# Optimization experiments

Measured on AMD Instinct MI355X. Metric: run time of the kernel, lower is better.

The kernel has to match this reference:

```python
import jax, jax.numpy as jnp
import numpy as np

NUM_CLASSES = [5, 7, 4, 6, 3, 8, 5, 4, 6, 7, 3, 5, 4, 6, 8, 5, 7, 4, 6, 3]
N_ONE_HOTS = 20
N_OTHERS = 30
H = 48
W = 48
B = 128
N_MAP = 32
ENC_OUT = 32
RES_C = 128
OH_EMB = 9
SUM_NC = sum(NUM_CLASSES)  # 106


def conv2d(x, w, b=None, pad=0):
    # x: NCHW, w: OIHW
    y = jax.lax.conv_general_dilated(
        x, w, window_strides=(1, 1), padding=[(pad, pad), (pad, pad)],
        dimension_numbers=('NCHW', 'OIHW', 'NCHW'))
    if b is not None:
        y = y + b[None, :, None, None]
    return y


def setup_inputs() -> dict:
    key = jax.random.key(0)
    ks = jax.random.split(key, 20)
    x = jax.random.normal(ks[0], (B, 1 + N_MAP, H, W), dtype=jnp.float32)
    # first N_ONE_HOTS entries of flattened channel 0 are categorical indices
    idx_cols = [jax.random.randint(jax.random.fold_in(ks[1], j), (B,), 0, nc)
                for j, nc in enumerate(NUM_CLASSES)]
    idx = jnp.stack(idx_cols, axis=1).astype(jnp.float32)  # (B, 20)
    x = x.at[:, 0, 0, :N_ONE_HOTS].set(idx)
    s = 0.05
    inp = {
        'x': x,
        'fc_w': jax.random.normal(ks[2], (OH_EMB, SUM_NC), jnp.float32) * s,
        'fc_b': jnp.zeros((OH_EMB,), jnp.float32),
        'oh_conv_w': jax.random.normal(ks[3], (OH_EMB, OH_EMB, 1, 1), jnp.float32) * s,
        'oh_conv_b': jnp.zeros((OH_EMB,), jnp.float32),
        'others_conv_w': jax.random.normal(ks[4], (N_OTHERS, N_OTHERS, 1, 1), jnp.float32) * s,
        'others_conv_b': jnp.zeros((N_OTHERS,), jnp.float32),
        'all_conv_w': jax.random.normal(ks[5], (ENC_OUT, OH_EMB + N_OTHERS, 1, 1), jnp.float32) * s,
        'all_conv_b': jnp.zeros((ENC_OUT,), jnp.float32),
        'conv1_w': jax.random.normal(ks[6], (RES_C, ENC_OUT + N_MAP, 1, 1), jnp.float32) * s,
        'conv1_b': jnp.zeros((RES_C,), jnp.float32),
        'rconv1_w': jax.random.normal(ks[7], (RES_C, RES_C, 5, 5), jnp.float32) * s,
        'rconv1_b': jnp.zeros((RES_C,), jnp.float32),
        'rconv2_w': jax.random.normal(ks[8], (RES_C, RES_C, 5, 5), jnp.float32) * s,
        'rconv2_b': jnp.zeros((RES_C,), jnp.float32),
        'se_w1': jax.random.normal(ks[9], (RES_C // 16, RES_C), jnp.float32) * s,
        'se_w2': jax.random.normal(ks[10], (RES_C, RES_C // 16), jnp.float32) * s,
    }
    return inp


def reference(x, fc_w, fc_b, oh_conv_w, oh_conv_b, others_conv_w, others_conv_b,
              all_conv_w, all_conv_b, conv1_w, conv1_b, rconv1_w, rconv1_b,
              rconv2_w, rconv2_b, se_w1, se_w2):
    b = x.shape[0]
    gi = x[:, 0].reshape(b, -1)                 # (b, H*W)
    map_feature = x[:, 1:]                      # (b, N_MAP, H, W)
    idx = jax.lax.stop_gradient(gi[:, :N_ONE_HOTS]).astype(jnp.int32)
    others = gi[:, N_ONE_HOTS:N_ONE_HOTS + N_OTHERS]   # (b, 30)
    # vectorized one-hot build (replaces the quadratic python loop)
    oh = jnp.concatenate(
        [jax.nn.one_hot(idx[:, j], nc, dtype=x.dtype) for j, nc in enumerate(NUM_CLASSES)],
        axis=1)                                 # (b, SUM_NC)
    v = oh @ fc_w.T + fc_b                      # (b, 9)
    # faithful torch expand((h,w)+shape).reshape((b,-1,h,w)) semantics
    v = jnp.broadcast_to(v, (H, W, b, OH_EMB)).reshape(b, OH_EMB, H, W)
    o = jnp.broadcast_to(others, (H, W, b, N_OTHERS)).reshape(b, N_OTHERS, H, W)
    v = conv2d(v, oh_conv_w, oh_conv_b)
    o = conv2d(o, others_conv_w, others_conv_b)
    gi_map = conv2d(jnp.concatenate([v, o], axis=1), all_conv_w, all_conv_b)  # (b, 32, H, W)
    h = conv2d(jnp.concatenate([gi_map, map_feature], axis=1), conv1_w, conv1_b)  # (b, 128, H, W)
    # residual block: 5x5 convs, LeakyReLU, SE, identity skip (in==out)
    identity = h
    y = jax.nn.leaky_relu(conv2d(h, rconv1_w, rconv1_b, pad=2))
    y = conv2d(y, rconv2_w, rconv2_b, pad=2)
    s = y.mean(axis=(2, 3))                     # (b, 128)
    s = jax.nn.sigmoid(jax.nn.relu(s @ se_w1.T) @ se_w2.T)
    y = y * s[:, :, None, None]
    return jax.nn.leaky_relu(y + identity)
```

## Files before the change

### kernel.cpp

```cpp
#include <hip/hip_runtime.h>
#include <hip/hip_bf16.h>
#include <cstddef>

#define HH 48
#define WW 48
#define PIX 2304
#define PPIX 2704
#define BB 128
#define RESC 128
#define XCH 33

typedef short bf16x8 __attribute__((ext_vector_type(8)));
typedef float f32x4 __attribute__((ext_vector_type(4)));

static __device__ __forceinline__ float b2f(unsigned short u) {
    unsigned x = ((unsigned)u) << 16;
    return __builtin_bit_cast(float, x);
}
static __device__ __forceinline__ unsigned short f2b(float f) {
    __hip_bfloat16 hb = __float2bfloat16(f);
    return __builtin_bit_cast(unsigned short, hb);
}

#define GLOAD_LDS16(gp, lp) __builtin_amdgcn_global_load_lds( \
    (const __attribute__((address_space(1))) void*)(gp), \
    (__attribute__((address_space(3))) void*)(lp), 16, 0, 0)

__global__ __launch_bounds__(256) void k_compute_G(
        const float* __restrict__ x, const float* __restrict__ fc_w,
        const float* __restrict__ fc_b,
        const float* __restrict__ ohw, const float* __restrict__ ohb,
        const float* __restrict__ otw, const float* __restrict__ otb,
        const float* __restrict__ aw,  const float* __restrict__ ab,
        const float* __restrict__ c1w, const float* __restrict__ c1b,
        float* __restrict__ G) {
    __shared__ float vsh[128][9];
    int t = threadIdx.x;
    if (t < 128) {
        const int off[20] = {0,5,12,16,22,25,33,38,42,48,55,58,63,67,73,81,86,93,97,103};
        const float* gi = x + (size_t)t * XCH * PIX;
        int cols[20];
        #pragma unroll
        for (int j = 0; j < 20; j++) cols[j] = off[j] + (int)gi[j];
        #pragma unroll
        for (int e = 0; e < 9; e++) {
            float acc = fc_b[e];
            #pragma unroll
            for (int j = 0; j < 20; j++) acc += fc_w[e * 106 + cols[j]];
            vsh[t][e] = acc;
        }
    }
    __syncthreads();
    int p = blockIdx.x * 64 + (t & 63);
    int og = t >> 6;
    if (p >= PIX) return;
    float sv = vsh[(p / 9) & 127][p % 9];
    float om[30];
    #pragma unroll
    for (int c2 = 0; c2 < 30; c2++) {
        int tmp = c2 * 24 + p;
        int c = tmp % 30;
        int bb = (c2 * 76 + tmp / 30) & 127;
        om[c2] = x[(size_t)bb * XCH * PIX + 20 + c];
    }
    float v9[9];
    #pragma unroll
    for (int e = 0; e < 9; e++) {
        float srow = 0.f;
        #pragma unroll
        for (int e2 = 0; e2 < 9; e2++) srow += ohw[e * 9 + e2];
        v9[e] = ohb[e] + srow * sv;
    }
    float o30[30];
    #pragma unroll
    for (int c = 0; c < 30; c++) {
        float a = otb[c];
        #pragma unroll
        for (int c2 = 0; c2 < 30; c2++) a += otw[c * 30 + c2] * om[c2];
        o30[c] = a;
    }
    float gi32[32];
    #pragma unroll
    for (int g = 0; g < 32; g++) {
        float a = ab[g];
        #pragma unroll
        for (int e = 0; e < 9; e++) a += aw[g * 39 + e] * v9[e];
        #pragma unroll
        for (int c = 0; c < 30; c++) a += aw[g * 39 + 9 + c] * o30[c];
        gi32[g] = a;
    }
    for (int oc = og * 32; oc < og * 32 + 32; oc++) {
        float a = c1b[oc];
        #pragma unroll
        for (int g = 0; g < 32; g++) a += c1w[oc * 64 + g] * gi32[g];
        G[p * 128 + oc] = a;
    }
}

__global__ void k_convert_w(const float* __restrict__ w1, const float* __restrict__ w2,
                            __hip_bfloat16* __restrict__ wb1, __hip_bfloat16* __restrict__ wb2) {
    int i = blockIdx.x * 256 + threadIdx.x;
    if (i >= 25 * 128 * 128) return;
    int tap = i / 16384, r = i % 16384;
    int oc = r >> 7, ic = r & 127;
    size_t src = (size_t)(oc * 128 + ic) * 25 + tap;
    wb1[i] = __float2bfloat16(w1[src]);
    wb2[i] = __float2bfloat16(w2[src]);
}

__global__ void k_zero_border(__hip_bfloat16* __restrict__ a, __hip_bfloat16* __restrict__ b2,
                              float* __restrict__ mean) {
    int img = blockIdx.x, t = threadIdx.x;
    if (t < 128) mean[img * 128 + t] = 0.f;
    for (int j = t; j < 6400; j += 256) {
        int pb = j >> 4, c16 = j & 15;
        int y, x2;
        if (pb < 208) { int q = pb / 52; y = q < 2 ? q : q + 48; x2 = pb % 52; }
        else { int r = pb - 208; y = 2 + (r >> 2); int c = r & 3; x2 = c < 2 ? c : c + 48; }
        size_t off = ((size_t)img * PPIX + y * 52 + x2) * 128 + c16 * 8;
        uint4 z = {0, 0, 0, 0};
        *(uint4*)(a + off) = z;
        *(uint4*)(b2 + off) = z;
    }
}

__global__ __launch_bounds__(256) void k_conv1(const float* __restrict__ x, const float* __restrict__ c1w,
                                               const float* __restrict__ G, __hip_bfloat16* __restrict__ h) {
    int b = blockIdx.y, p0 = blockIdx.x * 64;
    int t = threadIdx.x, wave = t >> 6, lane = t & 63;
    int l15 = lane & 15, lg = lane >> 4;

    bf16x8 a[2];
    #pragma unroll
    for (int m = 0; m < 2; ++m) {
        int oc = wave * 32 + m * 16 + l15;
        const float* wp = c1w + oc * 64 + 32 + lg * 8;
        float4 f0 = *(const float4*)wp;
        float4 f1 = *(const float4*)(wp + 4);
        unsigned short u[8] = { f2b(f0.x), f2b(f0.y), f2b(f0.z), f2b(f0.w),
                                f2b(f1.x), f2b(f1.y), f2b(f1.z), f2b(f1.w) };
        a[m] = __builtin_bit_cast(bf16x8, *(uint4*)u);
    }

    f32x4 acc[2][4] = {};
    #pragma unroll
    for (int n = 0; n < 4; ++n) {
        int p = p0 + n * 16 + l15;
        unsigned short ub[8];
        #pragma unroll
        for (int j = 0; j < 8; ++j)
            ub[j] = f2b(x[((size_t)b * XCH + 1 + lg * 8 + j) * PIX + p]);
        bf16x8 Bv = __builtin_bit_cast(bf16x8, *(uint4*)ub);
        acc[0][n] = __builtin_amdgcn_mfma_f32_16x16x32_bf16(a[0], Bv, acc[0][n], 0, 0, 0);
        acc[1][n] = __builtin_amdgcn_mfma_f32_16x16x32_bf16(a[1], Bv, acc[1][n], 0, 0, 0);
    }

    #pragma unroll
    for (int m = 0; m < 2; ++m) {
        #pragma unroll
        for (int n = 0; n < 4; ++n) {
            int oc4 = wave * 32 + m * 16 + lg * 4;
            int p = p0 + n * 16 + l15;
            int py = p / 48, px2 = p % 48;
            float4 g = *(const float4*)&G[(size_t)p * 128 + oc4];
            float v0 = acc[m][n][0] + g.x, v1 = acc[m][n][1] + g.y;
            float v2 = acc[m][n][2] + g.z, v3 = acc[m][n][3] + g.w;
            uint2 pk;
            pk.x = (unsigned)f2b(v0) | ((unsigned)f2b(v1) << 16);
            pk.y = (unsigned)f2b(v2) | ((unsigned)f2b(v3) << 16);
            *(uint2*)(&h[((size_t)b * PPIX + (py + 2) * 52 + px2 + 2) * 128 + oc4]) = pk;
        }
    }
}

template<bool LEAKY, bool MEAN, bool PADOUT>
__global__ __launch_bounds__(256, 2) void k_conv5_mfma(
        const __hip_bfloat16* __restrict__ in,
        const __hip_bfloat16* __restrict__ w,
        const float* __restrict__ bias,
        __hip_bfloat16* __restrict__ out,
        float* __restrict__ mean) {
    __shared__ __align__(16) char lds[2][25600];
    int bid = blockIdx.x;
    int xcd = bid & 7, loc = bid >> 3;
    int b = xcd * 16 + loc / 9;
    int tile = loc % 9;
    int ty0 = (tile / 3) * 16, tx0 = (tile % 3) * 16;
    int t = threadIdx.x;
    int wave = t >> 6, lane = t & 63;
    int wm = wave & 1, wn = wave >> 1;
    int l15 = lane & 15, lg = lane >> 4;

    const size_t inb = (size_t)b * PPIX * 128;
    const __hip_bfloat16* wbase = w + (size_t)(wm * 64 + l15) * 128 + lg * 8;

    int sbase[8];
    #pragma unroll
    for (int n = 0; n < 8; ++n) sbase[n] = (wn * 8 + n) * 20 + l15;

    f32x4 acc[4][8] = {};

    auto stage_part = [&](int buf, int icb2, int part) {
        int sg = part * 256 + t;
        if (sg < 1600) {
            int u = sg >> 3, j = sg & 7;
            int bb2 = j ^ (u & 7);
            int s = (u << 1) | (bb2 >> 2);
            int lg2 = bb2 & 3;
            int ry = s / 20, rx = s % 20;
            const __hip_bfloat16* gp = in + inb + (size_t)((ty0 + ry) * 52 + tx0 + rx) * 128 + icb2 + lg2 * 8;
            char* lp = &lds[buf][sg * 16];
            GLOAD_LDS16(gp, lp);
        }
    };

#define AISSUE(Areg, tap_) do { \
        const __hip_bfloat16* wp = wbase + (size_t)(tap_) * 16384 + icb; \
        Areg[0] = *(const bf16x8*)(wp); \
        Areg[1] = *(const bf16x8*)(wp + 2048); \
        Areg[2] = *(const bf16x8*)(wp + 4096); \
        Areg[3] = *(const bf16x8*)(wp + 6144); \
    } while (0)

#define LDSB(s_) (*(const bf16x8*)(cb + (((s_) >> 1) << 7) + \
        ((((((s_) & 1) << 2) | lg) ^ (((s_) >> 1) & 7)) << 4)))

#define CTAP(Areg, tap_) do { \
        int toff = (tap_) + 15 * ((tap_) / 5); \
        bf16x8 Bc0 = LDSB(sbase[0] + toff); \
        bf16x8 Bc1 = LDSB(sbase[1] + toff); \
        __builtin_amdgcn_s_setprio(1); \
        _Pragma("unroll") \
        for (int n = 0; n < 8; ++n) { \
            bf16x8 Bc2 = Bc1; \
            if (n < 6) Bc2 = LDSB(sbase[n + 2] + toff); \
            acc[0][n] = __builtin_amdgcn_mfma_f32_16x16x32_bf16(Areg[0], Bc0, acc[0][n], 0, 0, 0); \
            acc[1][n] = __builtin_amdgcn_mfma_f32_16x16x32_bf16(Areg[1], Bc0, acc[1][n], 0, 0, 0); \
            acc[2][n] = __builtin_amdgcn_mfma_f32_16x16x32_bf16(Areg[2], Bc0, acc[2][n], 0, 0, 0); \
            acc[3][n] = __builtin_amdgcn_mfma_f32_16x16x32_bf16(Areg[3], Bc0, acc[3][n], 0, 0, 0); \
            Bc0 = Bc1; Bc1 = Bc2; \
        } \
        __builtin_amdgcn_s_setprio(0); \
    } while (0)

    #pragma unroll
    for (int j = 0; j < 7; ++j) stage_part(0, 0, j);
    __syncthreads();

    for (int c = 0; c < 4; ++c) {
        const int icb = c * 32;
        const char* cb = lds[c & 1];
        bf16x8 A0[4], A1[4];
        AISSUE(A0, 0);
        AISSUE(A1, 1);
        __builtin_amdgcn_sched_barrier(0);
        for (int i = 0; i < 12; ++i) {
            int tp = 2 * i;
            CTAP(A0, tp);
            AISSUE(A0, tp + 2);
            if (c < 3 && i < 7) {
                stage_part((c + 1) & 1, icb + 32, i);
                __builtin_amdgcn_sched_barrier(0);
            }
            CTAP(A1, tp + 1);
            AISSUE(A1, tp + 3);
        }
        CTAP(A0, 24);
        if (c < 3) __syncthreads();
    }
#undef AISSUE
#undef LDSB
#undef CTAP

    #pragma unroll
    for (int m = 0; m < 4; ++m) {
        int ocm = wm * 64 + m * 16 + lg * 4;
        float bv0 = bias[ocm], bv1 = bias[ocm + 1], bv2 = bias[ocm + 2], bv3 = bias[ocm + 3];
        float ps0 = 0, ps1 = 0, ps2 = 0, ps3 = 0;
        #pragma unroll
        for (int n = 0; n < 8; ++n) {
            float v0 = acc[m][n][0] + bv0, v1 = acc[m][n][1] + bv1;
            float v2 = acc[m][n][2] + bv2, v3 = acc[m][n][3] + bv3;
            ps0 += v0; ps1 += v1; ps2 += v2; ps3 += v3;
            if (LEAKY) {
                v0 = v0 > 0.f ? v0 : 0.01f * v0; v1 = v1 > 0.f ? v1 : 0.01f * v1;
                v2 = v2 > 0.f ? v2 : 0.01f * v2; v3 = v3 > 0.f ? v3 : 0.01f * v3;
            }
            int row = ty0 + wn * 8 + n, col = tx0 + l15;
            size_t off;
            if (PADOUT) off = ((size_t)b * PPIX + (row + 2) * 52 + col + 2) * 128 + ocm;
            else        off = ((size_t)b * PIX + row * 48 + col) * 128 + ocm;
            uint2 pk;
            pk.x = (unsigned)f2b(v0) | ((unsigned)f2b(v1) << 16);
            pk.y = (unsigned)f2b(v2) | ((unsigned)f2b(v3) << 16);
            *(uint2*)(out + off) = pk;
        }
        if (MEAN) {
            #pragma unroll
            for (int mask = 1; mask < 16; mask <<= 1) {
                ps0 += __shfl_xor(ps0, mask);
                ps1 += __shfl_xor(ps1, mask);
                ps2 += __shfl_xor(ps2, mask);
                ps3 += __shfl_xor(ps3, mask);
            }
            if (l15 == 0) {
                atomicAdd(&mean[b * 128 + ocm], ps0);
                atomicAdd(&mean[b * 128 + ocm + 1], ps1);
                atomicAdd(&mean[b * 128 + ocm + 2], ps2);
                atomicAdd(&mean[b * 128 + ocm + 3], ps3);
            }
        }
    }
}

__global__ void k_se(const float* __restrict__ mean, const float* __restrict__ w1,
                     const float* __restrict__ w2, float* __restrict__ s) {
    __shared__ float m[128];
    __shared__ float tt[8];
    int b = blockIdx.x, t = threadIdx.x;
    m[t] = mean[b * RESC + t] * (1.0f / 2304.0f);
    __syncthreads();
    if (t < 8) {
        float a = 0.f;
        for (int i = 0; i < 128; i++) a += w1[t * 128 + i] * m[i];
        tt[t] = a > 0.f ? a : 0.f;
    }
    __syncthreads();
    float a = 0.f;
    #pragma unroll
    for (int r = 0; r < 8; r++) a += w2[t * 8 + r] * tt[r];
    s[b * RESC + t] = 1.f / (1.f + expf(-a));
}

__global__ __launch_bounds__(256) void k_final(const __hip_bfloat16* __restrict__ y2,
                                               const __hip_bfloat16* __restrict__ h,
                                               const float* __restrict__ sg, float* __restrict__ out) {
    __shared__ float sl[128];
    __shared__ float tile[64 * 129];
    int b = blockIdx.y, p0 = blockIdx.x * 64, t = threadIdx.x;
    if (t < 128) sl[t] = sg[b * 128 + t];
    __syncthreads();
    #pragma unroll
    for (int k = 0; k < 4; ++k) {
        int j = t + k * 256;
        int pix = j >> 4, c = j & 15;
        int p = p0 + pix;
        int py = p / 48, px2 = p % 48;
        uint4 yv = *(const uint4*)(y2 + ((size_t)b * PIX + p) * 128 + c * 8);
        uint4 hv = *(const uint4*)(h + ((size_t)b * PPIX + (py + 2) * 52 + px2 + 2) * 128 + c * 8);
        const unsigned short* yp = (const unsigned short*)&yv;
        const unsigned short* hp = (const unsigned short*)&hv;
        #pragma unroll
        for (int jj = 0; jj < 8; ++jj) {
            int oc = c * 8 + jj;
            tile[pix * 129 + oc] = b2f(yp[jj]) * sl[oc] + b2f(hp[jj]);
        }
    }
    __syncthreads();
    int oc = t >> 1, xh = (t & 1) * 32;
    float ov[32];
    #pragma unroll
    for (int i = 0; i < 32; ++i) {
        float v = tile[(xh + i) * 129 + oc];
        ov[i] = v > 0.f ? v : 0.01f * v;
    }
    float* op = out + ((size_t)b * 128 + oc) * PIX + p0 + xh;
    #pragma unroll
    for (int q = 0; q < 8; ++q) ((float4*)op)[q] = *(float4*)&ov[q * 4];
}

extern "C" void kernel_launch(void* const* d_in, const int* in_sizes, int n_in,
                              void* d_out, int out_size, void* d_ws, size_t ws_size,
                              hipStream_t stream) {
    const float* x      = (const float*)d_in[0];
    const float* fc_w   = (const float*)d_in[1];
    const float* fc_b   = (const float*)d_in[2];
    const float* ohw    = (const float*)d_in[3];
    const float* ohb    = (const float*)d_in[4];
    const float* otw    = (const float*)d_in[5];
    const float* otb    = (const float*)d_in[6];
    const float* aw     = (const float*)d_in[7];
    const float* ab     = (const float*)d_in[8];
    const float* c1w    = (const float*)d_in[9];
    const float* c1b    = (const float*)d_in[10];
    const float* r1w    = (const float*)d_in[11];
    const float* r1b    = (const float*)d_in[12];
    const float* r2w    = (const float*)d_in[13];
    const float* r2b    = (const float*)d_in[14];
    const float* se_w1  = (const float*)d_in[15];
    const float* se_w2  = (const float*)d_in[16];

    const size_t padb = (size_t)BB * PPIX * 128 * sizeof(__hip_bfloat16);
    char* ws = (char*)d_ws;
    __hip_bfloat16* h    = (__hip_bfloat16*)ws;  ws += padb;
    __hip_bfloat16* y1   = (__hip_bfloat16*)ws;  ws += padb;
    __hip_bfloat16* y2   = (__hip_bfloat16*)ws;  ws += (size_t)BB * PIX * 128 * sizeof(__hip_bfloat16);
    float* G    = (float*)ws;                    ws += (size_t)PIX * 128 * sizeof(float);
    __hip_bfloat16* wb1 = (__hip_bfloat16*)ws;   ws += (size_t)25 * 128 * 128 * sizeof(__hip_bfloat16);
    __hip_bfloat16* wb2 = (__hip_bfloat16*)ws;   ws += (size_t)25 * 128 * 128 * sizeof(__hip_bfloat16);
    ws += 262144;
    float* mean = (float*)ws;                    ws += (size_t)BB * RESC * sizeof(float);
    float* sgate= (float*)ws;                    ws += (size_t)BB * RESC * sizeof(float);

    k_compute_G<<<36, 256, 0, stream>>>(x, fc_w, fc_b, ohw, ohb, otw, otb, aw, ab, c1w, c1b, G);
    k_convert_w<<<1600, 256, 0, stream>>>(r1w, r2w, wb1, wb2);
    k_zero_border<<<128, 256, 0, stream>>>(h, y1, mean);
    k_conv1<<<dim3(36, 128), 256, 0, stream>>>(x, c1w, G, h);
    k_conv5_mfma<true, false, true><<<dim3(1152), 256, 0, stream>>>(h, wb1, r1b, y1, nullptr);
    k_conv5_mfma<false, true, false><<<dim3(1152), 256, 0, stream>>>(y1, wb2, r2b, y2, mean);
    k_se<<<128, 128, 0, stream>>>(mean, se_w1, se_w2, sgate);
    k_final<<<dim3(36, 128), 256, 0, stream>>>(y2, h, sgate, (float*)d_out);
}
```

Baseline: 726.2 us.

## Restructure 5x5 conv to 512 threads with full-input LDS staging and row-reuse loop

The 5x5 MFMA conv now runs 8 waves per block instead of 4, each wave covering 32 output channels and 8 rows. The whole 128-channel padded input tile (100KB) is staged into LDS once up front, replacing the double-buffered per-32-channel pipeline. The tap loop is reordered: for each dx, all five dy weight fragments are kept in registers, and every LDS row fragment feeds up to five output rows. This cuts LDS reads, but the single large LDS buffer limits occupancy and removes the overlap between staging and compute.

```diff
diff --git a/kernel.cpp b/kernel.cpp
--- a/kernel.cpp
+++ b/kernel.cpp
@@ -174,13 +174,13 @@
 }
 
 template<bool LEAKY, bool MEAN, bool PADOUT>
-__global__ __launch_bounds__(256, 2) void k_conv5_mfma(
+__global__ __launch_bounds__(512, 2) void k_conv5_mfma(
         const __hip_bfloat16* __restrict__ in,
         const __hip_bfloat16* __restrict__ w,
         const float* __restrict__ bias,
         __hip_bfloat16* __restrict__ out,
         float* __restrict__ mean) {
-    __shared__ __align__(16) char lds[2][25600];
+    __shared__ __align__(16) char lds[102400];
     int bid = blockIdx.x;
     int xcd = bid & 7, loc = bid >> 3;
     int b = xcd * 16 + loc / 9;
@@ -188,93 +188,76 @@
     int ty0 = (tile / 3) * 16, tx0 = (tile % 3) * 16;
     int t = threadIdx.x;
     int wave = t >> 6, lane = t & 63;
-    int wm = wave & 1, wn = wave >> 1;
+    int wm = wave & 3, wn = wave >> 2;
     int l15 = lane & 15, lg = lane >> 4;
 
     const size_t inb = (size_t)b * PPIX * 128;
-    const __hip_bfloat16* wbase = w + (size_t)(wm * 64 + l15) * 128 + lg * 8;
-
-    int sbase[8];
-    #pragma unroll
-    for (int n = 0; n < 8; ++n) sbase[n] = (wn * 8 + n) * 20 + l15;
-
-    f32x4 acc[4][8] = {};
-
-    auto stage_part = [&](int buf, int icb2, int part) {
-        int sg = part * 256 + t;
-        if (sg < 1600) {
-            int u = sg >> 3, j = sg & 7;
+    const __hip_bfloat16* wbase = w + (size_t)(wm * 32 + l15) * 128 + lg * 8;
+
+    f32x4 acc[2][8] = {};
+
+    #pragma unroll
+    for (int part = 0; part < 13; ++part) {
+        int sg = part * 512 + t;
+        if (sg < 6400) {
+            int plane = sg / 1600, r = sg % 1600;
+            int u = r >> 3, j = r & 7;
             int bb2 = j ^ (u & 7);
             int s = (u << 1) | (bb2 >> 2);
             int lg2 = bb2 & 3;
             int ry = s / 20, rx = s % 20;
-            const __hip_bfloat16* gp = in + inb + (size_t)((ty0 + ry) * 52 + tx0 + rx) * 128 + icb2 + lg2 * 8;
-            char* lp = &lds[buf][sg * 16];
+            const __hip_bfloat16* gp = in + inb + (size_t)((ty0 + ry) * 52 + tx0 + rx) * 128
+                                       + plane * 32 + lg2 * 8;
+            char* lp = &lds[plane * 25600 + r * 16];
             GLOAD_LDS16(gp, lp);
         }
-    };
-
-#define AISSUE(Areg, tap_) do { \
-        const __hip_bfloat16* wp = wbase + (size_t)(tap_) * 16384 + icb; \
-        Areg[0] = *(const bf16x8*)(wp); \
-        Areg[1] = *(const bf16x8*)(wp + 2048); \
-        Areg[2] = *(const bf16x8*)(wp + 4096); \
-        Areg[3] = *(const bf16x8*)(wp + 6144); \
-    } while (0)
+    }
+    __syncthreads();
 
 #define LDSB(s_) (*(const bf16x8*)(cb + (((s_) >> 1) << 7) + \
         ((((((s_) & 1) << 2) | lg) ^ (((s_) >> 1) & 7)) << 4)))
 
-#define CTAP(Areg, tap_) do { \
-        int toff = (tap_) + 15 * ((tap_) / 5); \
-        bf16x8 Bc0 = LDSB(sbase[0] + toff); \
-        bf16x8 Bc1 = LDSB(sbase[1] + toff); \
-        __builtin_amdgcn_s_setprio(1); \
-        _Pragma("unroll") \
-        for (int n = 0; n < 8; ++n) { \
-            bf16x8 Bc2 = Bc1; \
-            if (n < 6) Bc2 = LDSB(sbase[n + 2] + toff); \
-            acc[0][n] = __builtin_amdgcn_mfma_f32_16x16x32_bf16(Areg[0], Bc0, acc[0][n], 0, 0, 0); \
-            acc[1][n] = __builtin_amdgcn_mfma_f32_16x16x32_bf16(Areg[1], Bc0, acc[1][n], 0, 0, 0); \
-            acc[2][n] = __builtin_amdgcn_mfma_f32_16x16x32_bf16(Areg[2], Bc0, acc[2][n], 0, 0, 0); \
-            acc[3][n] = __builtin_amdgcn_mfma_f32_16x16x32_bf16(Areg[3], Bc0, acc[3][n], 0, 0, 0); \
-            Bc0 = Bc1; Bc1 = Bc2; \
-        } \
-        __builtin_amdgcn_s_setprio(0); \
-    } while (0)
-
-    #pragma unroll
-    for (int j = 0; j < 7; ++j) stage_part(0, 0, j);
-    __syncthreads();
-
+    const int s00 = wn * 160 + l15;
+
+    #pragma unroll 1
     for (int c = 0; c < 4; ++c) {
         const int icb = c * 32;
-        const char* cb = lds[c & 1];
-        bf16x8 A0[4], A1[4];
-        AISSUE(A0, 0);
-        AISSUE(A1, 1);
-        __builtin_amdgcn_sched_barrier(0);
-        for (int i = 0; i < 12; ++i) {
-            int tp = 2 * i;
-            CTAP(A0, tp);
-            AISSUE(A0, tp + 2);
-            if (c < 3 && i < 7) {
-                stage_part((c + 1) & 1, icb + 32, i);
-                __builtin_amdgcn_sched_barrier(0);
-            }
-            CTAP(A1, tp + 1);
-            AISSUE(A1, tp + 3);
-        }
-        CTAP(A0, 24);
-        if (c < 3) __syncthreads();
-    }
-#undef AISSUE
+        const char* cb = lds + c * 25600;
+        #pragma unroll
+        for (int dx = 0; dx < 5; ++dx) {
+            bf16x8 A[5][2];
+            #pragma unroll
+            for (int dy = 0; dy < 5; ++dy) {
+                const __hip_bfloat16* wp = wbase + (size_t)(dy * 5 + dx) * 16384 + icb;
+                A[dy][0] = *(const bf16x8*)(wp);
+                A[dy][1] = *(const bf16x8*)(wp + 2048);
+            }
+            __builtin_amdgcn_sched_barrier(0);
+            int s0 = s00 + dx;
+            bf16x8 Bc = LDSB(s0);
+            __builtin_amdgcn_s_setprio(1);
+            #pragma unroll
+            for (int r = 0; r < 12; ++r) {
+                bf16x8 Bn = Bc;
+                if (r < 11) Bn = LDSB(s0 + (r + 1) * 20);
+                #pragma unroll
+                for (int dy = 0; dy < 5; ++dy) {
+                    const int n = r - dy;
+                    if (n >= 0 && n < 8) {
+                        acc[0][n] = __builtin_amdgcn_mfma_f32_16x16x32_bf16(A[dy][0], Bc, acc[0][n], 0, 0, 0);
+                        acc[1][n] = __builtin_amdgcn_mfma_f32_16x16x32_bf16(A[dy][1], Bc, acc[1][n], 0, 0, 0);
+                    }
+                }
+                Bc = Bn;
+            }
+            __builtin_amdgcn_s_setprio(0);
+        }
+    }
 #undef LDSB
-#undef CTAP
-
-    #pragma unroll
-    for (int m = 0; m < 4; ++m) {
-        int ocm = wm * 64 + m * 16 + lg * 4;
+
+    #pragma unroll
+    for (int m = 0; m < 2; ++m) {
+        int ocm = wm * 32 + m * 16 + lg * 4;
         float bv0 = bias[ocm], bv1 = bias[ocm + 1], bv2 = bias[ocm + 2], bv3 = bias[ocm + 3];
         float ps0 = 0, ps1 = 0, ps2 = 0, ps3 = 0;
         #pragma unroll
@@ -406,8 +389,8 @@
     k_convert_w<<<1600, 256, 0, stream>>>(r1w, r2w, wb1, wb2);
     k_zero_border<<<128, 256, 0, stream>>>(h, y1, mean);
     k_conv1<<<dim3(36, 128), 256, 0, stream>>>(x, c1w, G, h);
-    k_conv5_mfma<true, false, true><<<dim3(1152), 256, 0, stream>>>(h, wb1, r1b, y1, nullptr);
-    k_conv5_mfma<false, true, false><<<dim3(1152), 256, 0, stream>>>(y1, wb2, r2b, y2, mean);
+    k_conv5_mfma<true, false, true><<<dim3(1152), 512, 0, stream>>>(h, wb1, r1b, y1, nullptr);
+    k_conv5_mfma<false, true, false><<<dim3(1152), 512, 0, stream>>>(y1, wb2, r2b, y2, mean);
     k_se<<<128, 128, 0, stream>>>(mean, se_w1, se_w2, sgate);
     k_final<<<dim3(36, 128), 256, 0, stream>>>(y2, h, sgate, (float*)d_out);
 }
```

Result: no change. 731.2 us, median of 2 (+0.7%).
